# Optimization experiments

Hardware: AMD Instinct MI355X
Metric: run time of the kernel (lower is better)

## Reference

```python
import jax, jax.numpy as jnp
import numpy as np
import math

DIM = 1024
N_HEADS = 16
HEAD_DIM = DIM // N_HEADS
BS, SEQ, NNB = 8, 1024, 50
LN_EPS = 1e-12


def setup_inputs() -> dict:
    key = jax.random.key(0)
    ks = jax.random.split(key, 12)
    std = 0.02
    inp = {
        "x": jax.random.normal(ks[0], (BS, SEQ, DIM), jnp.float32),
        "x_neighbor": jax.random.normal(ks[1], (BS, NNB, DIM), jnp.float32),
        "mask": jnp.ones((BS, SEQ), jnp.int32),
        "neighbor_mask": jnp.ones((BS, NNB), jnp.float32),
        "qw": std * jax.random.normal(ks[2], (DIM, DIM), jnp.float32),
        "qb": jnp.zeros((DIM,), jnp.float32),
        "kw": std * jax.random.normal(ks[3], (DIM, DIM), jnp.float32),
        "kb": jnp.zeros((DIM,), jnp.float32),
        "vw": std * jax.random.normal(ks[4], (DIM, DIM), jnp.float32),
        "vb": jnp.zeros((DIM,), jnp.float32),
        "ow": std * jax.random.normal(ks[5], (DIM, DIM), jnp.float32),
        "ob": jnp.zeros((DIM,), jnp.float32),
        "ln_g": jnp.ones((DIM,), jnp.float32),
        "ln_b": jnp.zeros((DIM,), jnp.float32),
    }
    return inp


def _split_heads(t, bs):
    # [bs, s, dim] -> [bs, h, s, dh]
    return t.reshape(bs, -1, N_HEADS, HEAD_DIM).transpose(0, 2, 1, 3)


def reference(x, x_neighbor, mask, neighbor_mask, qw, qb, kw, kb, vw, vb, ow, ob, ln_g, ln_b):
    bs, seq, dim = x.shape
    # mean-pool neighbors with mask
    nm = neighbor_mask[..., None]                      # [bs, nnb, 1]
    xn = (x_neighbor * nm).sum(axis=1) / nm.sum(axis=1)  # [bs, dim]
    query = jnp.broadcast_to(xn[:, None, :], x.shape)    # [bs, seq, dim]

    q = _split_heads(query @ qw.T + qb, bs) / math.sqrt(HEAD_DIM)
    k = _split_heads(x @ kw.T + kb, bs)
    v = _split_heads(x @ vw.T + vb, bs)

    scores = jnp.einsum("bhqd,bhkd->bhqk", q, k)       # [bs, h, seq, seq]
    key_mask = (mask == 0)[:, None, None, :]            # [bs, 1, 1, seq]
    scores = jnp.where(key_mask, -jnp.inf, scores)
    weights = jax.nn.softmax(scores, axis=-1)           # dropout p=0.0 -> no-op
    context = jnp.einsum("bhqk,bhkd->bhqd", weights, v)
    context = context.transpose(0, 2, 1, 3).reshape(bs, seq, dim)
    out = context @ ow.T + ob

    h = out + x
    mu = h.mean(axis=-1, keepdims=True)
    var = ((h - mu) ** 2).mean(axis=-1, keepdims=True)
    return (h - mu) / jnp.sqrt(var + LN_EPS) * ln_g + ln_b
```

## Files before the change

kernel.cpp:

```cpp
#include <hip/hip_runtime.h>
#include <hip/hip_bf16.h>


#define DIM  1024
#define NH   16
#define HD   64
#define BS   8
#define SEQ  1024
#define NNB  50

__global__ void k_zero(float* __restrict__ buf){
  int i = blockIdx.x*1024 + threadIdx.x;
  #pragma unroll
  for (int k=0; k<4; k++) buf[i + 256*k] = 0.f;
}

__global__ void k_pool(const float* __restrict__ xnb, const float* __restrict__ nm,
                       float* __restrict__ xn){
  int b = blockIdx.x;
  int d = threadIdx.x*4;
  float4 acc = {0,0,0,0}; float wsum = 0.f;
  for (int n=0; n<NNB; n++){
    float w = nm[b*NNB + n];
    float4 v = *(const float4*)(xnb + (size_t)(b*NNB + n)*DIM + d);
    acc.x += w*v.x; acc.y += w*v.y; acc.z += w*v.z; acc.w += w*v.w;
    wsum += w;
  }
  float inv = 1.f/wsum;
  acc.x*=inv; acc.y*=inv; acc.z*=inv; acc.w*=inv;
  *(float4*)(xn + b*DIM + d) = acc;
}

__global__ void k_q(const float* __restrict__ xn, const float* __restrict__ qw,
                    const float* __restrict__ qb, float* __restrict__ q){
  int wv = threadIdx.x >> 6, ln = threadIdx.x & 63;
  int j = blockIdx.x*4 + wv;
  float acc[BS] = {0,0,0,0,0,0,0,0};
  #pragma unroll
  for (int i=0; i<4; i++){
    int d = ln*4 + 256*i;
    float4 wt = *(const float4*)(qw + (size_t)j*DIM + d);
    #pragma unroll
    for (int b=0; b<BS; b++){
      float4 xv = *(const float4*)(xn + b*DIM + d);
      acc[b] += wt.x*xv.x + wt.y*xv.y + wt.z*xv.z + wt.w*xv.w;
    }
  }
  #pragma unroll
  for (int off=32; off>=1; off>>=1){
    #pragma unroll
    for (int b=0; b<BS; b++) acc[b] += __shfl_down(acc[b], off, 64);
  }
  if (ln == 0){
    float bias = qb[j];
    #pragma unroll
    for (int b=0; b<BS; b++) q[b*DIM + j] = (acc[b] + bias) * 0.125f;
  }
}

__global__ void k_p(const float* __restrict__ q, const float* __restrict__ kw,
                    float* __restrict__ p){
  int dc = blockIdx.x, h = blockIdx.y, b = blockIdx.z;
  int d = dc*256 + threadIdx.x;
  const float* qrow = q + b*DIM + h*HD;
  float acc = 0.f;
  #pragma unroll 8
  for (int j=0; j<HD; j++)
    acc += qrow[j] * kw[(size_t)(h*HD + j)*DIM + d];
  p[(size_t)(b*NH + h)*DIM + d] = acc;
}

__global__ void k_scores(const float* __restrict__ x, const float* __restrict__ p,
                         float* __restrict__ sc){
  int s0 = blockIdx.x * 64;
  int b  = blockIdx.y;
  int kbase = blockIdx.z * 256;
  int tid = threadIdx.x;
  __shared__ float4 plds[256*5];
  __shared__ float  xlds[64*68];
  float* pf = (float*)plds;
  #pragma unroll
  for (int it=0; it<16; it++){
    int idx = it*256 + tid;
    int d = idx & 255, h = idx >> 8;
    pf[d*20 + h] = p[(size_t)(b*NH + h)*DIM + kbase + d];
  }
  int s = tid & 63, g = tid >> 6;
  float acc[4] = {0.f,0.f,0.f,0.f};
  for (int dk=0; dk<4; dk++){
    __syncthreads();
    #pragma unroll
    for (int it=0; it<4; it++){
      int idx = it*256 + tid;
      int dd4 = idx & 15, ss = idx >> 4;
      float4 v = *(const float4*)(x + (size_t)(b*SEQ + s0 + ss)*DIM + kbase + dk*64 + dd4*4);
      *(float4*)(xlds + ss*68 + dd4*4) = v;
    }
    __syncthreads();
    #pragma unroll 4
    for (int dd4=0; dd4<16; dd4++){
      float4 xq = *(const float4*)(xlds + s*68 + dd4*4);
      int dbase = (dk*64 + dd4*4)*5 + g;
      float4 p0 = plds[dbase], p1 = plds[dbase+5], p2 = plds[dbase+10], p3 = plds[dbase+15];
      acc[0] += xq.x*p0.x + xq.y*p1.x + xq.z*p2.x + xq.w*p3.x;
      acc[1] += xq.x*p0.y + xq.y*p1.y + xq.z*p2.y + xq.w*p3.y;
      acc[2] += xq.x*p0.z + xq.y*p1.z + xq.z*p2.z + xq.w*p3.z;
      acc[3] += xq.x*p0.w + xq.y*p1.w + xq.z*p2.w + xq.w*p3.w;
    }
  }
  #pragma unroll
  for (int u=0; u<4; u++)
    atomicAdd(&sc[(size_t)(b*NH + g*4 + u)*SEQ + s0 + s], acc[u]);
}

__global__ void k_softmax(float* __restrict__ sc, const int* __restrict__ mask){
  int b = blockIdx.x >> 4, h = blockIdx.x & 15;
  int tid = threadIdx.x;
  float v[4];
  float mx = -3e38f;
  #pragma unroll
  for (int i=0; i<4; i++){
    int s = tid + 256*i;
    float v0 = sc[(size_t)(b*NH + h)*SEQ + s];
    if (mask[b*SEQ + s] == 0) v0 = -1e30f;
    v[i] = v0;
    mx = fmaxf(mx, v0);
  }
  #pragma unroll
  for (int off=32; off>=1; off>>=1) mx = fmaxf(mx, __shfl_xor(mx, off, 64));
  __shared__ float r1[4], r2[4];
  int wv = tid >> 6, ln = tid & 63;
  if (ln == 0) r1[wv] = mx;
  __syncthreads();
  mx = fmaxf(fmaxf(r1[0], r1[1]), fmaxf(r1[2], r1[3]));
  float sum = 0.f;
  #pragma unroll
  for (int i=0; i<4; i++){ v[i] = __expf(v[i] - mx); sum += v[i]; }
  #pragma unroll
  for (int off=32; off>=1; off>>=1) sum += __shfl_xor(sum, off, 64);
  if (ln == 0) r2[wv] = sum;
  __syncthreads();
  sum = r2[0] + r2[1] + r2[2] + r2[3];
  float inv = 1.f / sum;
  #pragma unroll
  for (int i=0; i<4; i++) sc[(size_t)(b*NH + h)*SEQ + tid + 256*i] = v[i] * inv;
}

__global__ void k_wpool(const float* __restrict__ x, const float* __restrict__ w,
                        float* __restrict__ xw){
  int dc = blockIdx.x, b = blockIdx.y, scn = blockIdx.z;
  int tid = threadIdx.x;
  __shared__ float4 wlds[64*5];
  float* wf = (float*)wlds;
  #pragma unroll
  for (int it=0; it<4; it++){
    int idx = it*256 + tid;
    int ss = idx >> 4, hh = idx & 15;
    wf[ss*20 + hh] = w[(size_t)(b*NH + hh)*SEQ + scn*64 + ss];
  }
  __syncthreads();
  int ln = tid & 63, wv = tid >> 6;
  int d = dc*256 + ln*4;
  float4 a0={0,0,0,0}, a1={0,0,0,0}, a2={0,0,0,0}, a3={0,0,0,0};
  #pragma unroll 4
  for (int s=0; s<64; s++){
    float4 xq = *(const float4*)(x + (size_t)(b*SEQ + scn*64 + s)*DIM + d);
    float4 wq = wlds[s*5 + wv];
    a0.x+=xq.x*wq.x; a0.y+=xq.y*wq.x; a0.z+=xq.z*wq.x; a0.w+=xq.w*wq.x;
    a1.x+=xq.x*wq.y; a1.y+=xq.y*wq.y; a1.z+=xq.z*wq.y; a1.w+=xq.w*wq.y;
    a2.x+=xq.x*wq.z; a2.y+=xq.y*wq.z; a2.z+=xq.z*wq.z; a2.w+=xq.w*wq.z;
    a3.x+=xq.x*wq.w; a3.y+=xq.y*wq.w; a3.z+=xq.z*wq.w; a3.w+=xq.w*wq.w;
  }
  float4 a[4] = {a0,a1,a2,a3};
  #pragma unroll
  for (int u=0; u<4; u++){
    float* dst = xw + (size_t)(b*NH + wv*4 + u)*DIM + d;
    atomicAdd(dst+0, a[u].x); atomicAdd(dst+1, a[u].y);
    atomicAdd(dst+2, a[u].z); atomicAdd(dst+3, a[u].w);
  }
}

__global__ void k_ctx(const float* __restrict__ xw, const float* __restrict__ vw,
                      const float* __restrict__ vb, float* __restrict__ ctx){
  int wv = threadIdx.x >> 6, ln = threadIdx.x & 63;
  int jo = blockIdx.x*4 + wv;
  int h  = jo >> 6;
  float acc[BS] = {0,0,0,0,0,0,0,0};
  #pragma unroll
  for (int i=0; i<4; i++){
    int d = ln*4 + 256*i;
    float4 vv = *(const float4*)(vw + (size_t)jo*DIM + d);
    #pragma unroll
    for (int b=0; b<BS; b++){
      float4 xv = *(const float4*)(xw + (size_t)(b*NH + h)*DIM + d);
      acc[b] += vv.x*xv.x + vv.y*xv.y + vv.z*xv.z + vv.w*xv.w;
    }
  }
  #pragma unroll
  for (int off=32; off>=1; off>>=1){
    #pragma unroll
    for (int b=0; b<BS; b++) acc[b] += __shfl_down(acc[b], off, 64);
  }
  if (ln == 0){
    float bias = vb[jo];
    #pragma unroll
    for (int b=0; b<BS; b++) ctx[b*DIM + jo] = acc[b] + bias;
  }
}

__global__ void k_outrow(const float* __restrict__ ctx, const float* __restrict__ ow,
                         const float* __restrict__ ob, float* __restrict__ outr){
  int wv = threadIdx.x >> 6, ln = threadIdx.x & 63;
  int io = blockIdx.x*4 + wv;
  float acc[BS] = {0,0,0,0,0,0,0,0};
  #pragma unroll
  for (int i=0; i<4; i++){
    int d = ln*4 + 256*i;
    float4 wt = *(const float4*)(ow + (size_t)io*DIM + d);
    #pragma unroll
    for (int b=0; b<BS; b++){
      float4 cv = *(const float4*)(ctx + b*DIM + d);
      acc[b] += wt.x*cv.x + wt.y*cv.y + wt.z*cv.z + wt.w*cv.w;
    }
  }
  #pragma unroll
  for (int off=32; off>=1; off>>=1){
    #pragma unroll
    for (int b=0; b<BS; b++) acc[b] += __shfl_down(acc[b], off, 64);
  }
  if (ln == 0){
    float bias = ob[io];
    #pragma unroll
    for (int b=0; b<BS; b++) outr[b*DIM + io] = acc[b] + bias;
  }
}

__global__ void k_ln(const float* __restrict__ x, const float* __restrict__ outr,
                     const float* __restrict__ g, const float* __restrict__ bt,
                     float* __restrict__ out){
  int row = blockIdx.x;
  int b = row >> 10;
  size_t base = (size_t)row * DIM;
  int tid = threadIdx.x;
  float4 xv = ((const float4*)(x + base))[tid];
  float4 ov = ((const float4*)(outr + (size_t)b*DIM))[tid];
  float4 h;
  h.x = xv.x + ov.x; h.y = xv.y + ov.y; h.z = xv.z + ov.z; h.w = xv.w + ov.w;
  float s  = h.x + h.y + h.z + h.w;
  float s2 = h.x*h.x + h.y*h.y + h.z*h.z + h.w*h.w;
  #pragma unroll
  for (int off=32; off>=1; off>>=1){
    s  += __shfl_xor(s,  off, 64);
    s2 += __shfl_xor(s2, off, 64);
  }
  __shared__ float r1[4], r2[4];
  int wv = tid >> 6, ln = tid & 63;
  if (ln == 0){ r1[wv] = s; r2[wv] = s2; }
  __syncthreads();
  s  = r1[0] + r1[1] + r1[2] + r1[3];
  s2 = r2[0] + r2[1] + r2[2] + r2[3];
  float mu   = s  * (1.f/1024.f);
  float var  = s2 * (1.f/1024.f) - mu*mu;
  float rstd = rsqrtf(var + 1e-12f);
  float4 gv = ((const float4*)g)[tid];
  float4 bv = ((const float4*)bt)[tid];
  float4 y;
  y.x = (h.x - mu)*rstd*gv.x + bv.x;
  y.y = (h.y - mu)*rstd*gv.y + bv.y;
  y.z = (h.z - mu)*rstd*gv.z + bv.z;
  y.w = (h.w - mu)*rstd*gv.w + bv.w;
  ((float4*)(out + base))[tid] = y;
}

extern "C" void kernel_launch(void* const* d_in, const int* in_sizes, int n_in,
                              void* d_out, int out_size, void* d_ws, size_t ws_size,
                              hipStream_t stream) {
  const float* x    = (const float*)d_in[0];
  const float* xnb  = (const float*)d_in[1];
  const int*   mask = (const int*  )d_in[2];
  const float* nm   = (const float*)d_in[3];
  const float* qw   = (const float*)d_in[4];
  const float* qb   = (const float*)d_in[5];
  const float* kw   = (const float*)d_in[6];
  const float* vw   = (const float*)d_in[8];
  const float* vb   = (const float*)d_in[9];
  const float* ow   = (const float*)d_in[10];
  const float* ob   = (const float*)d_in[11];
  const float* lng  = (const float*)d_in[12];
  const float* lnb  = (const float*)d_in[13];
  float* out = (float*)d_out;

  float* ws   = (float*)d_ws;
  float* xn   = ws;
  float* q    = ws + 8192;
  float* p    = ws + 16384;
  float* sc   = ws + 147456;
  float* xw   = ws + 278528;
  float* ctx  = ws + 409600;
  float* outr = ws + 417792;

  k_zero   <<<256,             256, 0, stream>>>(sc);
  k_pool   <<<BS,              256, 0, stream>>>(xnb, nm, xn);
  k_q      <<<256,             256, 0, stream>>>(xn, qw, qb, q);
  k_p      <<<dim3(4,NH,BS),   256, 0, stream>>>(q, kw, p);
  k_scores <<<dim3(16,BS,4),   256, 0, stream>>>(x, p, sc);
  k_softmax<<<BS*NH,           256, 0, stream>>>(sc, mask);
  k_wpool  <<<dim3(4,BS,16),   256, 0, stream>>>(x, sc, xw);
  k_ctx    <<<256,             256, 0, stream>>>(xw, vw, vb, ctx);
  k_outrow <<<256,             256, 0, stream>>>(ctx, ow, ob, outr);
  k_ln     <<<BS*SEQ,          256, 0, stream>>>(x, outr, lng, lnb, out);
}
```

Before: 199.3 us.

## Fuse scores, softmax and weighted pooling into one split-sequence attention kernel

Replaces the separate score, softmax and weighted-pool kernels, their atomics and the zeroing kernel with one kernel per 32-row sequence chunk and batch. Each block computes full-depth scores for its rows and exponentiates them under the mask. It writes per-chunk numerator slabs and denominators, which a small reduction kernel sums and divides. This removes atomic contention, two global round trips of the score matrix and several launches, at the cost of a 16 MB partial buffer. Dropping the max subtraction also risks exp overflow for large scores.

```diff
diff --git a/kernel.cpp b/kernel.cpp
--- a/kernel.cpp
+++ b/kernel.cpp
@@ -9,17 +9,12 @@
 #define SEQ  1024
 #define NNB  50
 
-__global__ void k_zero(float* __restrict__ buf){
-  int i = blockIdx.x*1024 + threadIdx.x;
-  #pragma unroll
-  for (int k=0; k<4; k++) buf[i + 256*k] = 0.f;
-}
-
 __global__ void k_pool(const float* __restrict__ xnb, const float* __restrict__ nm,
                        float* __restrict__ xn){
   int b = blockIdx.x;
   int d = threadIdx.x*4;
   float4 acc = {0,0,0,0}; float wsum = 0.f;
+  #pragma unroll 10
   for (int n=0; n<NNB; n++){
     float w = nm[b*NNB + n];
     float4 v = *(const float4*)(xnb + (size_t)(b*NNB + n)*DIM + d);
@@ -70,114 +65,125 @@
   p[(size_t)(b*NH + h)*DIM + d] = acc;
 }
 
-__global__ void k_scores(const float* __restrict__ x, const float* __restrict__ p,
-                         float* __restrict__ sc){
-  int s0 = blockIdx.x * 64;
+__global__ void k_att(const float* __restrict__ x, const float* __restrict__ p,
+                      const int* __restrict__ mask,
+                      float* __restrict__ nump, float* __restrict__ denp){
+  int sc = blockIdx.x;
   int b  = blockIdx.y;
-  int kbase = blockIdx.z * 256;
+  int s0 = sc * 32;
   int tid = threadIdx.x;
   __shared__ float4 plds[256*5];
-  __shared__ float  xlds[64*68];
+  __shared__ float  xlds[32*68];
+  __shared__ float4 elds[32*5];
   float* pf = (float*)plds;
-  #pragma unroll
-  for (int it=0; it<16; it++){
-    int idx = it*256 + tid;
-    int d = idx & 255, h = idx >> 8;
-    pf[d*20 + h] = p[(size_t)(b*NH + h)*DIM + kbase + d];
-  }
-  int s = tid & 63, g = tid >> 6;
-  float acc[4] = {0.f,0.f,0.f,0.f};
-  for (int dk=0; dk<4; dk++){
+  float* ef = (float*)elds;
+  int ln = tid & 63, g = tid >> 6;
+  int sA = ln & 15, qr = ln >> 4;
+  float accA[4] = {0,0,0,0}, accB[4] = {0,0,0,0};
+  for (int kc=0; kc<4; kc++){
+    int kbase = kc*256;
     __syncthreads();
     #pragma unroll
-    for (int it=0; it<4; it++){
+    for (int it=0; it<16; it++){
       int idx = it*256 + tid;
-      int dd4 = idx & 15, ss = idx >> 4;
-      float4 v = *(const float4*)(x + (size_t)(b*SEQ + s0 + ss)*DIM + kbase + dk*64 + dd4*4);
-      *(float4*)(xlds + ss*68 + dd4*4) = v;
-    }
-    __syncthreads();
+      int d = idx & 255, h = idx >> 8;
+      pf[d*20 + h] = p[(size_t)(b*NH + h)*DIM + kbase + d];
+    }
+    for (int dk=0; dk<4; dk++){
+      __syncthreads();
+      #pragma unroll
+      for (int it=0; it<2; it++){
+        int idx = it*256 + tid;
+        int dd4 = idx & 15, ss = idx >> 4;
+        float4 v = *(const float4*)(x + (size_t)(b*SEQ + s0 + ss)*DIM + kbase + dk*64 + dd4*4);
+        *(float4*)(xlds + ss*68 + dd4*4) = v;
+      }
+      __syncthreads();
+      #pragma unroll
+      for (int j=0; j<4; j++){
+        int dd4 = qr*4 + j;
+        float4 xa = *(const float4*)(xlds + sA*68 + dd4*4);
+        float4 xb = *(const float4*)(xlds + (sA+16)*68 + dd4*4);
+        int dbase = (dk*64 + dd4*4)*5 + g;
+        float4 p0 = plds[dbase], p1 = plds[dbase+5], p2 = plds[dbase+10], p3 = plds[dbase+15];
+        accA[0] += xa.x*p0.x + xa.y*p1.x + xa.z*p2.x + xa.w*p3.x;
+        accA[1] += xa.x*p0.y + xa.y*p1.y + xa.z*p2.y + xa.w*p3.y;
+        accA[2] += xa.x*p0.z + xa.y*p1.z + xa.z*p2.z + xa.w*p3.z;
+        accA[3] += xa.x*p0.w + xa.y*p1.w + xa.z*p2.w + xa.w*p3.w;
+        accB[0] += xb.x*p0.x + xb.y*p1.x + xb.z*p2.x + xb.w*p3.x;
+        accB[1] += xb.x*p0.y + xb.y*p1.y + xb.z*p2.y + xb.w*p3.y;
+        accB[2] += xb.x*p0.z + xb.y*p1.z + xb.z*p2.z + xb.w*p3.z;
+        accB[3] += xb.x*p0.w + xb.y*p1.w + xb.z*p2.w + xb.w*p3.w;
+      }
+    }
+  }
+  #pragma unroll
+  for (int u=0; u<4; u++){
+    accA[u] += __shfl_xor(accA[u], 16, 64);
+    accA[u] += __shfl_xor(accA[u], 32, 64);
+    accB[u] += __shfl_xor(accB[u], 16, 64);
+    accB[u] += __shfl_xor(accB[u], 32, 64);
+  }
+  int mA = mask[b*SEQ + s0 + sA];
+  int mB = mask[b*SEQ + s0 + sA + 16];
+  float eA[4], eB[4];
+  #pragma unroll
+  for (int u=0; u<4; u++){
+    eA[u] = mA ? __expf(accA[u]) : 0.f;
+    eB[u] = mB ? __expf(accB[u]) : 0.f;
+  }
+  if (qr == 0){
+    #pragma unroll
+    for (int u=0; u<4; u++){
+      ef[sA*20 + g*4 + u]      = eA[u];
+      ef[(sA+16)*20 + g*4 + u] = eB[u];
+    }
+  }
+  float dsum[4];
+  #pragma unroll
+  for (int u=0; u<4; u++) dsum[u] = eA[u] + eB[u];
+  #pragma unroll
+  for (int off=8; off>=1; off>>=1){
+    #pragma unroll
+    for (int u=0; u<4; u++) dsum[u] += __shfl_xor(dsum[u], off, 64);
+  }
+  if (ln == 0){
+    #pragma unroll
+    for (int u=0; u<4; u++) denp[(sc*BS + b)*NH + g*4 + u] = dsum[u];
+  }
+  __syncthreads();
+  float* nslab = nump + (size_t)sc*(BS*NH*DIM) + (size_t)(b*NH + g*4)*DIM;
+  const float* xrow0 = x + (size_t)(b*SEQ + s0)*DIM;
+  for (int r=0; r<4; r++){
+    int dbase = r*256 + ln*4;
+    float4 a0={0,0,0,0}, a1={0,0,0,0}, a2={0,0,0,0}, a3={0,0,0,0};
     #pragma unroll 4
-    for (int dd4=0; dd4<16; dd4++){
-      float4 xq = *(const float4*)(xlds + s*68 + dd4*4);
-      int dbase = (dk*64 + dd4*4)*5 + g;
-      float4 p0 = plds[dbase], p1 = plds[dbase+5], p2 = plds[dbase+10], p3 = plds[dbase+15];
-      acc[0] += xq.x*p0.x + xq.y*p1.x + xq.z*p2.x + xq.w*p3.x;
-      acc[1] += xq.x*p0.y + xq.y*p1.y + xq.z*p2.y + xq.w*p3.y;
-      acc[2] += xq.x*p0.z + xq.y*p1.z + xq.z*p2.z + xq.w*p3.z;
-      acc[3] += xq.x*p0.w + xq.y*p1.w + xq.z*p2.w + xq.w*p3.w;
-    }
-  }
-  #pragma unroll
-  for (int u=0; u<4; u++)
-    atomicAdd(&sc[(size_t)(b*NH + g*4 + u)*SEQ + s0 + s], acc[u]);
-}
-
-__global__ void k_softmax(float* __restrict__ sc, const int* __restrict__ mask){
-  int b = blockIdx.x >> 4, h = blockIdx.x & 15;
-  int tid = threadIdx.x;
-  float v[4];
-  float mx = -3e38f;
-  #pragma unroll
-  for (int i=0; i<4; i++){
-    int s = tid + 256*i;
-    float v0 = sc[(size_t)(b*NH + h)*SEQ + s];
-    if (mask[b*SEQ + s] == 0) v0 = -1e30f;
-    v[i] = v0;
-    mx = fmaxf(mx, v0);
-  }
-  #pragma unroll
-  for (int off=32; off>=1; off>>=1) mx = fmaxf(mx, __shfl_xor(mx, off, 64));
-  __shared__ float r1[4], r2[4];
-  int wv = tid >> 6, ln = tid & 63;
-  if (ln == 0) r1[wv] = mx;
-  __syncthreads();
-  mx = fmaxf(fmaxf(r1[0], r1[1]), fmaxf(r1[2], r1[3]));
-  float sum = 0.f;
-  #pragma unroll
-  for (int i=0; i<4; i++){ v[i] = __expf(v[i] - mx); sum += v[i]; }
-  #pragma unroll
-  for (int off=32; off>=1; off>>=1) sum += __shfl_xor(sum, off, 64);
-  if (ln == 0) r2[wv] = sum;
-  __syncthreads();
-  sum = r2[0] + r2[1] + r2[2] + r2[3];
-  float inv = 1.f / sum;
-  #pragma unroll
-  for (int i=0; i<4; i++) sc[(size_t)(b*NH + h)*SEQ + tid + 256*i] = v[i] * inv;
-}
-
-__global__ void k_wpool(const float* __restrict__ x, const float* __restrict__ w,
-                        float* __restrict__ xw){
-  int dc = blockIdx.x, b = blockIdx.y, scn = blockIdx.z;
-  int tid = threadIdx.x;
-  __shared__ float4 wlds[64*5];
-  float* wf = (float*)wlds;
-  #pragma unroll
-  for (int it=0; it<4; it++){
-    int idx = it*256 + tid;
-    int ss = idx >> 4, hh = idx & 15;
-    wf[ss*20 + hh] = w[(size_t)(b*NH + hh)*SEQ + scn*64 + ss];
-  }
-  __syncthreads();
-  int ln = tid & 63, wv = tid >> 6;
-  int d = dc*256 + ln*4;
-  float4 a0={0,0,0,0}, a1={0,0,0,0}, a2={0,0,0,0}, a3={0,0,0,0};
-  #pragma unroll 4
-  for (int s=0; s<64; s++){
-    float4 xq = *(const float4*)(x + (size_t)(b*SEQ + scn*64 + s)*DIM + d);
-    float4 wq = wlds[s*5 + wv];
-    a0.x+=xq.x*wq.x; a0.y+=xq.y*wq.x; a0.z+=xq.z*wq.x; a0.w+=xq.w*wq.x;
-    a1.x+=xq.x*wq.y; a1.y+=xq.y*wq.y; a1.z+=xq.z*wq.y; a1.w+=xq.w*wq.y;
-    a2.x+=xq.x*wq.z; a2.y+=xq.y*wq.z; a2.z+=xq.z*wq.z; a2.w+=xq.w*wq.z;
-    a3.x+=xq.x*wq.w; a3.y+=xq.y*wq.w; a3.z+=xq.z*wq.w; a3.w+=xq.w*wq.w;
-  }
-  float4 a[4] = {a0,a1,a2,a3};
-  #pragma unroll
-  for (int u=0; u<4; u++){
-    float* dst = xw + (size_t)(b*NH + wv*4 + u)*DIM + d;
-    atomicAdd(dst+0, a[u].x); atomicAdd(dst+1, a[u].y);
-    atomicAdd(dst+2, a[u].z); atomicAdd(dst+3, a[u].w);
-  }
+    for (int s=0; s<32; s++){
+      float4 xv = *(const float4*)(xrow0 + (size_t)s*DIM + dbase);
+      float4 e4 = elds[s*5 + g];
+      a0.x+=xv.x*e4.x; a0.y+=xv.y*e4.x; a0.z+=xv.z*e4.x; a0.w+=xv.w*e4.x;
+      a1.x+=xv.x*e4.y; a1.y+=xv.y*e4.y; a1.z+=xv.z*e4.y; a1.w+=xv.w*e4.y;
+      a2.x+=xv.x*e4.z; a2.y+=xv.y*e4.z; a2.z+=xv.z*e4.z; a2.w+=xv.w*e4.z;
+      a3.x+=xv.x*e4.w; a3.y+=xv.y*e4.w; a3.z+=xv.z*e4.w; a3.w+=xv.w*e4.w;
+    }
+    *(float4*)(nslab            + dbase) = a0;
+    *(float4*)(nslab +   DIM    + dbase) = a1;
+    *(float4*)(nslab + 2*(size_t)DIM + dbase) = a2;
+    *(float4*)(nslab + 3*(size_t)DIM + dbase) = a3;
+  }
+}
+
+__global__ void k_attred(const float* __restrict__ nump, const float* __restrict__ denp,
+                         float* __restrict__ xw){
+  int id = blockIdx.x*256 + threadIdx.x;
+  int bh = id >> 10;
+  float den = 0.f;
+  #pragma unroll
+  for (int c=0; c<32; c++) den += denp[c*(BS*NH) + bh];
+  float v = 0.f;
+  #pragma unroll
+  for (int c=0; c<32; c++) v += nump[(size_t)c*(BS*NH*DIM) + id];
+  xw[id] = v / den;
 }
 
 __global__ void k_ctx(const float* __restrict__ xw, const float* __restrict__ vw,
@@ -294,18 +300,17 @@
   float* xn   = ws;
   float* q    = ws + 8192;
   float* p    = ws + 16384;
-  float* sc   = ws + 147456;
-  float* xw   = ws + 278528;
-  float* ctx  = ws + 409600;
-  float* outr = ws + 417792;
-
-  k_zero   <<<256,             256, 0, stream>>>(sc);
+  float* nump = ws + 147456;
+  float* denp = ws + 4341760;
+  float* xw   = ws + 4345856;
+  float* ctx  = ws + 4476928;
+  float* outr = ws + 4485120;
+
   k_pool   <<<BS,              256, 0, stream>>>(xnb, nm, xn);
   k_q      <<<256,             256, 0, stream>>>(xn, qw, qb, q);
   k_p      <<<dim3(4,NH,BS),   256, 0, stream>>>(q, kw, p);
-  k_scores <<<dim3(16,BS,4),   256, 0, stream>>>(x, p, sc);
-  k_softmax<<<BS*NH,           256, 0, stream>>>(sc, mask);
-  k_wpool  <<<dim3(4,BS,16),   256, 0, stream>>>(x, sc, xw);
+  k_att    <<<dim3(32,BS),     256, 0, stream>>>(x, p, mask, nump, denp);
+  k_attred <<<512,             256, 0, stream>>>(nump, denp, xw);
   k_ctx    <<<256,             256, 0, stream>>>(xw, vw, vb, ctx);
   k_outrow <<<256,             256, 0, stream>>>(ctx, ow, ob, outr);
   k_ln     <<<BS*SEQ,          256, 0, stream>>>(x, outr, lng, lnb, out);
```

New measurement: 302.2 us. 1.52x slower.
